# Kernel optimization log

Hardware: AMD Instinct MI355X
Metric: run time of the kernel (lower is better)

The kernel has to match this reference:

```python
import jax, jax.numpy as jnp
import numpy as np

B, S, D = 4, 4096, 768
E, SLOTS = 16, 1  # n_experts, slots_per_expert
H = 4 * D


def setup_inputs() -> dict:
    key = jax.random.key(0)
    k = jax.random.split(key, 6)
    scale1 = 1.0 / np.sqrt(D)
    scale2 = 1.0 / np.sqrt(H)
    return {
        "x": jax.random.normal(k[0], (B, S, D), dtype=jnp.float32),
        "phi": jax.random.normal(k[1], (D, E * SLOTS), dtype=jnp.float32),
        "W1": jax.random.normal(k[2], (E, D, H), dtype=jnp.float32) * scale1,
        "b1": jnp.zeros((E, H), dtype=jnp.float32),
        "W2": jax.random.normal(k[3], (E, H, D), dtype=jnp.float32) * scale2,
        "b2": jnp.zeros((E, D), dtype=jnp.float32),
    }


def reference(x, phi, W1, b1, W2, b2):
    # logits: [B, S, E*SLOTS]
    logits = jnp.einsum("bsd,dn->bsn", x, phi)
    dispatch_weights = jax.nn.softmax(logits, axis=-1)  # over slots
    combine_weights = jax.nn.softmax(logits, axis=1)    # over sequence
    # xs: [B, E*SLOTS, D] = dispatch^T @ x
    xs = jnp.einsum("bsn,bsd->bnd", dispatch_weights, x)
    xs = xs.reshape(B, E, SLOTS, D)
    # per-expert FFN, batched over experts: GELU (exact, as torch nn.GELU default)
    h = jnp.einsum("bepd,edh->beph", xs, W1) + b1[None, :, None, :]
    h = jax.nn.gelu(h, approximate=False)
    ys = jnp.einsum("beph,ehd->bepd", h, W2) + b2[None, :, None, :]
    ys = ys.reshape(B, E * SLOTS, D)
    # combine: [B, S, D]
    y = jnp.einsum("bsn,bnd->bsd", combine_weights, ys)
    return y
```

## Files before the change

kernel.cpp:

```cpp
#include <hip/hip_runtime.h>
#include <math.h>

constexpr int B = 4, S = 4096, D = 768, E = 16, N = 16, H = 3072;
constexpr int SCH = 32;
constexpr int NSCH = S / SCH;
constexpr int DL = 24;
constexpr int NDC = D / DL;
constexpr int HL2 = 96;
constexpr int NHC2 = H / HL2;
constexpr int LBLK = 32;
constexpr int LPB = S / LBLK;

constexpr size_t OFF_LOG  = 0;
constexpr size_t OFF_DW   = OFF_LOG + (size_t)B * S * N;
constexpr size_t OFF_PCM  = OFF_DW + (size_t)B * S * N;
constexpr size_t OFF_PCS  = OFF_PCM + (size_t)B * LPB * N;
constexpr size_t OFF_CMAX = OFF_PCS + (size_t)B * LPB * N;
constexpr size_t OFF_CSUM = OFF_CMAX + (size_t)B * N;
constexpr size_t OFF_XSP  = OFF_CSUM + (size_t)B * N;
constexpr size_t OFF_XS   = OFF_XSP + (size_t)B * NSCH * N * D;
constexpr size_t OFF_HP   = OFF_XS + (size_t)B * N * D;
constexpr size_t OFF_HACT = OFF_HP + (size_t)NDC * B * E * H;
constexpr size_t OFF_YSP  = OFF_HACT + (size_t)B * E * H;
constexpr size_t OFF_YS   = OFF_YSP + (size_t)NHC2 * B * E * D;

__device__ __forceinline__ void fma4(float4& a, float s, const float4& w) {
    a.x = fmaf(s, w.x, a.x);
    a.y = fmaf(s, w.y, a.y);
    a.z = fmaf(s, w.z, a.z);
    a.w = fmaf(s, w.w, a.w);
}

__global__ __launch_bounds__(256) void k_logits(const float* __restrict__ x,
                                                const float* __restrict__ phi,
                                                float* __restrict__ logits,
                                                float* __restrict__ dw,
                                                float* __restrict__ pcm,
                                                float* __restrict__ pcs) {
    __shared__ float ph[16][D];
    __shared__ float rm[16][16], rs[16][16];
    const int t = threadIdx.x;
    const int blk = blockIdx.x;
    const int b = blk / LPB;
    const int s0 = (blk % LPB) * LBLK;

#pragma unroll
    for (int i = 0; i < 12; ++i) {
        const int idx = i * 1024 + t * 4;
        const float4 v = *reinterpret_cast<const float4*>(phi + idx);
        const int d0 = idx >> 4;
        const int n0 = idx & 15;
        ph[n0 + 0][d0] = v.x;
        ph[n0 + 1][d0] = v.y;
        ph[n0 + 2][d0] = v.z;
        ph[n0 + 3][d0] = v.w;
    }
    __syncthreads();

    const int gid = t >> 4;
    const int ln = t & 15;
    const int s = s0 + gid * 2;
    const float* xr0 = x + ((size_t)b * S + s) * D;
    const float* xr1 = xr0 + D;

    float4 a0[12], a1[12];
#pragma unroll
    for (int j = 0; j < 12; ++j) {
        a0[j] = *reinterpret_cast<const float4*>(xr0 + j * 64 + ln * 4);
        a1[j] = *reinterpret_cast<const float4*>(xr1 + j * 64 + ln * 4);
    }
    float p0[16], p1[16];
#pragma unroll
    for (int n = 0; n < 16; ++n) {
        float q0 = 0.f, q1 = 0.f;
#pragma unroll
        for (int j = 0; j < 12; ++j) {
            const float4 pv = *reinterpret_cast<const float4*>(&ph[n][j * 64 + ln * 4]);
            q0 = fmaf(a0[j].x, pv.x, q0); q1 = fmaf(a1[j].x, pv.x, q1);
            q0 = fmaf(a0[j].y, pv.y, q0); q1 = fmaf(a1[j].y, pv.y, q1);
            q0 = fmaf(a0[j].z, pv.z, q0); q1 = fmaf(a1[j].z, pv.z, q1);
            q0 = fmaf(a0[j].w, pv.w, q0); q1 = fmaf(a1[j].w, pv.w, q1);
        }
        p0[n] = q0; p1[n] = q1;
    }
#pragma unroll
    for (int m = 1; m < 16; m <<= 1) {
#pragma unroll
        for (int n = 0; n < 16; ++n) {
            p0[n] += __shfl_xor(p0[n], m, 64);
            p1[n] += __shfl_xor(p1[n], m, 64);
        }
    }
    float m0 = -1e30f, m1 = -1e30f;
#pragma unroll
    for (int n = 0; n < 16; ++n) { m0 = fmaxf(m0, p0[n]); m1 = fmaxf(m1, p1[n]); }
    float su0 = 0.f, su1 = 0.f;
#pragma unroll
    for (int n = 0; n < 16; ++n) { su0 += __expf(p0[n] - m0); su1 += __expf(p1[n] - m1); }
    const size_t o0 = ((size_t)b * S + s) * N + ln;
    logits[o0] = p0[ln];
    logits[o0 + N] = p1[ln];
    dw[o0] = __expf(p0[ln] - m0) / su0;
    dw[o0 + N] = __expf(p1[ln] - m1) / su1;

    const float mm = fmaxf(p0[ln], p1[ln]);
    const float ss = __expf(p0[ln] - mm) + __expf(p1[ln] - mm);
    rm[gid][ln] = mm;
    rs[gid][ln] = ss;
    __syncthreads();
    if (t < 16) {
        float M = -1e30f;
#pragma unroll
        for (int g = 0; g < 16; ++g) M = fmaxf(M, rm[g][t]);
        float SS = 0.f;
#pragma unroll
        for (int g = 0; g < 16; ++g) SS += rs[g][t] * __expf(rm[g][t] - M);
        pcm[blk * 16 + t] = M;
        pcs[blk * 16 + t] = SS;
    }
}

__global__ __launch_bounds__(192) void k_xsp(const float* __restrict__ x,
                                             const float* __restrict__ dw,
                                             float* __restrict__ xsp) {
    const int blk = blockIdx.x;
    const int b = blk / NSCH;
    const int c = blk % NSCH;
    const int t = threadIdx.x;
    const int d = t * 4;
    float4 a[16];
#pragma unroll
    for (int n = 0; n < 16; ++n) a[n] = float4{0.f, 0.f, 0.f, 0.f};
    const float* xb = x + ((size_t)b * S + (size_t)c * SCH) * D + d;
    const float* dwb = dw + ((size_t)b * S + (size_t)c * SCH) * N;
#pragma unroll 2
    for (int s = 0; s < SCH; ++s) {
        const float4 xv = *reinterpret_cast<const float4*>(xb + (size_t)s * D);
#pragma unroll
        for (int n = 0; n < 16; ++n) {
            const float w = dwb[s * N + n];
            a[n].x = fmaf(w, xv.x, a[n].x);
            a[n].y = fmaf(w, xv.y, a[n].y);
            a[n].z = fmaf(w, xv.z, a[n].z);
            a[n].w = fmaf(w, xv.w, a[n].w);
        }
    }
    float* o = xsp + (size_t)blk * N * D + d;
#pragma unroll
    for (int n = 0; n < 16; ++n)
        *reinterpret_cast<float4*>(o + (size_t)n * D) = a[n];
}

__global__ __launch_bounds__(256) void k_xsred_cmerge(const float* __restrict__ xsp,
                                                      float* __restrict__ xs,
                                                      const float* __restrict__ pcm,
                                                      const float* __restrict__ pcs,
                                                      float* __restrict__ cmax,
                                                      float* __restrict__ csum) {
    const int t = threadIdx.x;
    if (blockIdx.x < 192) {
        const int i = blockIdx.x * 256 + t;
        const int b = i / (N * D);
        const int rem = i % (N * D);
        const float* p = xsp + (size_t)b * NSCH * N * D + rem;
        float sum = 0.f;
#pragma unroll 4
        for (int c = 0; c < NSCH; ++c) sum += p[(size_t)c * N * D];
        xs[i] = sum;
    } else if (t < 64) {
        const int b = t >> 4, n = t & 15;
        float M = -1e30f;
#pragma unroll 8
        for (int c = 0; c < LPB; ++c) M = fmaxf(M, pcm[((size_t)b * LPB + c) * 16 + n]);
        float SS = 0.f;
#pragma unroll 8
        for (int c = 0; c < LPB; ++c)
            SS += pcs[((size_t)b * LPB + c) * 16 + n] * __expf(pcm[((size_t)b * LPB + c) * 16 + n] - M);
        cmax[b * 16 + n] = M;
        csum[b * 16 + n] = SS;
    }
}

__global__ __launch_bounds__(256) void k_ffn1(const float* __restrict__ xs,
                                              const float* __restrict__ W1,
                                              float* __restrict__ hp) {
    __shared__ __align__(16) float xs_lds[DL][4];
    const int t = threadIdx.x;
    const int e = blockIdx.x / NDC;
    const int dc = blockIdx.x % NDC;
    const int d0 = dc * DL;
    if (t < DL * 4) {
        const int dd = t >> 2, b = t & 3;
        xs_lds[dd][b] = xs[((size_t)b * N + e) * D + d0 + dd];
    }
    __syncthreads();

    float4 acc[3][4];
#pragma unroll
    for (int k = 0; k < 3; ++k)
#pragma unroll
        for (int b = 0; b < 4; ++b) acc[k][b] = float4{0.f, 0.f, 0.f, 0.f};

    const float* wbase = W1 + ((size_t)e * D + d0) * H + t * 4;
#pragma unroll 4
    for (int dd = 0; dd < DL; ++dd) {
        const float4 xv = *reinterpret_cast<const float4*>(&xs_lds[dd][0]);
        const float* wrow = wbase + (size_t)dd * H;
        float4 w[3];
        w[0] = *reinterpret_cast<const float4*>(wrow);
        w[1] = *reinterpret_cast<const float4*>(wrow + 1024);
        w[2] = *reinterpret_cast<const float4*>(wrow + 2048);
#pragma unroll
        for (int k = 0; k < 3; ++k) {
            fma4(acc[k][0], xv.x, w[k]);
            fma4(acc[k][1], xv.y, w[k]);
            fma4(acc[k][2], xv.z, w[k]);
            fma4(acc[k][3], xv.w, w[k]);
        }
    }
#pragma unroll
    for (int k = 0; k < 3; ++k)
#pragma unroll
        for (int b = 0; b < 4; ++b)
            *reinterpret_cast<float4*>(hp + (((size_t)dc * 4 + b) * E + e) * H + k * 1024 + t * 4) = acc[k][b];
}

__global__ __launch_bounds__(256) void k_gelu(const float* __restrict__ hp,
                                              const float* __restrict__ b1,
                                              float* __restrict__ hact) {
    const int i4 = blockIdx.x * 256 + threadIdx.x;
    const int rem4 = i4 % (E * H / 4);
    float4 v = *reinterpret_cast<const float4*>(b1 + (size_t)rem4 * 4);
#pragma unroll 8
    for (int dc = 0; dc < NDC; ++dc) {
        const float4 p = *reinterpret_cast<const float4*>(hp + (size_t)dc * B * E * H + (size_t)i4 * 4);
        v.x += p.x; v.y += p.y; v.z += p.z; v.w += p.w;
    }
    float4 g;
    g.x = 0.5f * v.x * (1.0f + erff(v.x * 0.70710678118654752f));
    g.y = 0.5f * v.y * (1.0f + erff(v.y * 0.70710678118654752f));
    g.z = 0.5f * v.z * (1.0f + erff(v.z * 0.70710678118654752f));
    g.w = 0.5f * v.w * (1.0f + erff(v.w * 0.70710678118654752f));
    *reinterpret_cast<float4*>(hact + (size_t)i4 * 4) = g;
}

__global__ __launch_bounds__(192) void k_ffn2(const float* __restrict__ hact,
                                              const float* __restrict__ W2,
                                              float* __restrict__ ysp) {
    __shared__ __align__(16) float h_lds[HL2][4];
    const int t = threadIdx.x;
    const int e = blockIdx.x / NHC2;
    const int hc = blockIdx.x % NHC2;
    const int h0 = hc * HL2;
    for (int idx = t; idx < HL2 * 4; idx += 192) {
        const int hh = idx >> 2, b = idx & 3;
        h_lds[hh][b] = hact[((size_t)b * E + e) * H + h0 + hh];
    }
    __syncthreads();

    float4 acc[4];
#pragma unroll
    for (int b = 0; b < 4; ++b) acc[b] = float4{0.f, 0.f, 0.f, 0.f};

    const float* wbase = W2 + ((size_t)e * H + h0) * D + t * 4;
#pragma unroll 8
    for (int kk = 0; kk < HL2; ++kk) {
        const float4 hv = *reinterpret_cast<const float4*>(&h_lds[kk][0]);
        const float4 w = *reinterpret_cast<const float4*>(wbase + (size_t)kk * D);
        fma4(acc[0], hv.x, w);
        fma4(acc[1], hv.y, w);
        fma4(acc[2], hv.z, w);
        fma4(acc[3], hv.w, w);
    }
#pragma unroll
    for (int b = 0; b < 4; ++b)
        *reinterpret_cast<float4*>(ysp + (((size_t)hc * 4 + b) * E + e) * D + t * 4) = acc[b];
}

__global__ __launch_bounds__(256) void k_ysred(const float* __restrict__ ysp,
                                               const float* __restrict__ b2,
                                               float* __restrict__ ys) {
    const int i4 = blockIdx.x * 256 + threadIdx.x;
    const int rem4 = i4 % (E * D / 4);
    float4 v = *reinterpret_cast<const float4*>(b2 + (size_t)rem4 * 4);
#pragma unroll 8
    for (int hc = 0; hc < NHC2; ++hc) {
        const float4 u = *reinterpret_cast<const float4*>(ysp + (size_t)hc * B * E * D + (size_t)i4 * 4);
        v.x += u.x; v.y += u.y; v.z += u.z; v.w += u.w;
    }
    *reinterpret_cast<float4*>(ys + (size_t)i4 * 4) = v;
}

__global__ __launch_bounds__(192) void k_combine(const float* __restrict__ logits,
                                                 const float* __restrict__ cmax,
                                                 const float* __restrict__ csum,
                                                 const float* __restrict__ ys,
                                                 float* __restrict__ y) {
    const int blk = blockIdx.x;
    const int b = blk / (S / 8);
    const int s0 = (blk % (S / 8)) * 8;
    const int t = threadIdx.x;
    const int d4 = t * 4;

    float4 ysr[16];
    float cm[16], ci[16];
#pragma unroll
    for (int n = 0; n < 16; ++n) {
        ysr[n] = *reinterpret_cast<const float4*>(ys + ((size_t)b * N + n) * D + d4);
        cm[n] = cmax[b * N + n];
        ci[n] = 1.0f / csum[b * N + n];
    }
#pragma unroll
    for (int r = 0; r < 8; ++r) {
        const int s = s0 + r;
        const float* lrow = logits + ((size_t)b * S + s) * N;
        float4 acc{0, 0, 0, 0};
#pragma unroll
        for (int n = 0; n < 16; ++n) {
            const float cw = __expf(lrow[n] - cm[n]) * ci[n];
            acc.x = fmaf(cw, ysr[n].x, acc.x);
            acc.y = fmaf(cw, ysr[n].y, acc.y);
            acc.z = fmaf(cw, ysr[n].z, acc.z);
            acc.w = fmaf(cw, ysr[n].w, acc.w);
        }
        *reinterpret_cast<float4*>(y + ((size_t)b * S + s) * D + d4) = acc;
    }
}

extern "C" void kernel_launch(void* const* d_in, const int* in_sizes, int n_in,
                              void* d_out, int out_size, void* d_ws, size_t ws_size,
                              hipStream_t stream) {
    const float* x   = (const float*)d_in[0];
    const float* phi = (const float*)d_in[1];
    const float* W1  = (const float*)d_in[2];
    const float* b1  = (const float*)d_in[3];
    const float* W2  = (const float*)d_in[4];
    const float* b2  = (const float*)d_in[5];
    float* y = (float*)d_out;
    float* ws = (float*)d_ws;

    float* logits = ws + OFF_LOG;
    float* dw     = ws + OFF_DW;
    float* pcm    = ws + OFF_PCM;
    float* pcs    = ws + OFF_PCS;
    float* cmax   = ws + OFF_CMAX;
    float* csum   = ws + OFF_CSUM;
    float* xsp    = ws + OFF_XSP;
    float* xs     = ws + OFF_XS;
    float* hp     = ws + OFF_HP;
    float* hact   = ws + OFF_HACT;
    float* ysp    = ws + OFF_YSP;
    float* ys     = ws + OFF_YS;

    k_logits<<<B * LPB, 256, 0, stream>>>(x, phi, logits, dw, pcm, pcs);
    k_xsp<<<B * NSCH, 192, 0, stream>>>(x, dw, xsp);
    k_xsred_cmerge<<<193, 256, 0, stream>>>(xsp, xs, pcm, pcs, cmax, csum);
    k_ffn1<<<E * NDC, 256, 0, stream>>>(xs, W1, hp);
    k_gelu<<<(B * E * H / 4) / 256, 256, 0, stream>>>(hp, b1, hact);
    k_ffn2<<<E * NHC2, 192, 0, stream>>>(hact, W2, ysp);
    k_ysred<<<(B * E * D / 4) / 256, 256, 0, stream>>>(ysp, b2, ys);
    k_combine<<<B * (S / 8), 192, 0, stream>>>(logits, cmax, csum, ys, y);
}
```

Before: 171.2 us.

## Fuse hidden partial-sum reduction and GELU into FFN2, retile FFN1 over columns

Removes the standalone GELU kernel by having each FFN2 block reduce the FFN1 partial sums for its hidden slice, add the bias, apply exact GELU and stage the result in LDS. FFN1 now splits each expert's hidden columns into three blocks and uses a larger D chunk, so there are fewer partial sums to reduce and each thread holds fewer accumulators. FFN2 uses a smaller hidden chunk, which means more blocks and more ys partials, and the ys reduction loop is unrolled further. This saves a launch and the hact write/read round trip, but the hp partials are now read inside FFN2 and the ysp reduction has twice as much to sum.

```diff
diff --git a/kernel.cpp b/kernel.cpp
--- a/kernel.cpp
+++ b/kernel.cpp
@@ -4,9 +4,10 @@
 constexpr int B = 4, S = 4096, D = 768, E = 16, N = 16, H = 3072;
 constexpr int SCH = 32;
 constexpr int NSCH = S / SCH;
-constexpr int DL = 24;
-constexpr int NDC = D / DL;
-constexpr int HL2 = 96;
+constexpr int DL1 = 48;
+constexpr int NDC = D / DL1;
+constexpr int NHH = 3;
+constexpr int HL2 = 48;
 constexpr int NHC2 = H / HL2;
 constexpr int LBLK = 32;
 constexpr int LPB = S / LBLK;
@@ -20,8 +21,7 @@
 constexpr size_t OFF_XSP  = OFF_CSUM + (size_t)B * N;
 constexpr size_t OFF_XS   = OFF_XSP + (size_t)B * NSCH * N * D;
 constexpr size_t OFF_HP   = OFF_XS + (size_t)B * N * D;
-constexpr size_t OFF_HACT = OFF_HP + (size_t)NDC * B * E * H;
-constexpr size_t OFF_YSP  = OFF_HACT + (size_t)B * E * H;
+constexpr size_t OFF_YSP  = OFF_HP + (size_t)NDC * B * E * H;
 constexpr size_t OFF_YS   = OFF_YSP + (size_t)NHC2 * B * E * D;
 
 __device__ __forceinline__ void fma4(float4& a, float s, const float4& w) {
@@ -184,77 +184,59 @@
 __global__ __launch_bounds__(256) void k_ffn1(const float* __restrict__ xs,
                                               const float* __restrict__ W1,
                                               float* __restrict__ hp) {
-    __shared__ __align__(16) float xs_lds[DL][4];
-    const int t = threadIdx.x;
-    const int e = blockIdx.x / NDC;
-    const int dc = blockIdx.x % NDC;
-    const int d0 = dc * DL;
-    if (t < DL * 4) {
+    __shared__ __align__(16) float xs_lds[DL1][4];
+    const int t = threadIdx.x;
+    const int e = blockIdx.x / (NDC * NHH);
+    const int rem = blockIdx.x % (NDC * NHH);
+    const int dc = rem / NHH;
+    const int hh = rem % NHH;
+    const int d0 = dc * DL1;
+    const int col = hh * 1024 + t * 4;
+
+    if (t < DL1 * 4) {
         const int dd = t >> 2, b = t & 3;
         xs_lds[dd][b] = xs[((size_t)b * N + e) * D + d0 + dd];
     }
     __syncthreads();
 
-    float4 acc[3][4];
-#pragma unroll
-    for (int k = 0; k < 3; ++k)
-#pragma unroll
-        for (int b = 0; b < 4; ++b) acc[k][b] = float4{0.f, 0.f, 0.f, 0.f};
-
-    const float* wbase = W1 + ((size_t)e * D + d0) * H + t * 4;
-#pragma unroll 4
-    for (int dd = 0; dd < DL; ++dd) {
+    float4 acc[4];
+#pragma unroll
+    for (int b = 0; b < 4; ++b) acc[b] = float4{0.f, 0.f, 0.f, 0.f};
+
+    const float* wp = W1 + ((size_t)e * D + d0) * H + col;
+#pragma unroll 8
+    for (int dd = 0; dd < DL1; ++dd) {
+        const float4 w = *reinterpret_cast<const float4*>(wp + (size_t)dd * H);
         const float4 xv = *reinterpret_cast<const float4*>(&xs_lds[dd][0]);
-        const float* wrow = wbase + (size_t)dd * H;
-        float4 w[3];
-        w[0] = *reinterpret_cast<const float4*>(wrow);
-        w[1] = *reinterpret_cast<const float4*>(wrow + 1024);
-        w[2] = *reinterpret_cast<const float4*>(wrow + 2048);
-#pragma unroll
-        for (int k = 0; k < 3; ++k) {
-            fma4(acc[k][0], xv.x, w[k]);
-            fma4(acc[k][1], xv.y, w[k]);
-            fma4(acc[k][2], xv.z, w[k]);
-            fma4(acc[k][3], xv.w, w[k]);
-        }
-    }
-#pragma unroll
-    for (int k = 0; k < 3; ++k)
-#pragma unroll
-        for (int b = 0; b < 4; ++b)
-            *reinterpret_cast<float4*>(hp + (((size_t)dc * 4 + b) * E + e) * H + k * 1024 + t * 4) = acc[k][b];
-}
-
-__global__ __launch_bounds__(256) void k_gelu(const float* __restrict__ hp,
+        fma4(acc[0], xv.x, w);
+        fma4(acc[1], xv.y, w);
+        fma4(acc[2], xv.z, w);
+        fma4(acc[3], xv.w, w);
+    }
+#pragma unroll
+    for (int b = 0; b < 4; ++b)
+        *reinterpret_cast<float4*>(hp + (((size_t)dc * 4 + b) * E + e) * H + col) = acc[b];
+}
+
+__global__ __launch_bounds__(192) void k_ffn2(const float* __restrict__ hp,
                                               const float* __restrict__ b1,
-                                              float* __restrict__ hact) {
-    const int i4 = blockIdx.x * 256 + threadIdx.x;
-    const int rem4 = i4 % (E * H / 4);
-    float4 v = *reinterpret_cast<const float4*>(b1 + (size_t)rem4 * 4);
-#pragma unroll 8
-    for (int dc = 0; dc < NDC; ++dc) {
-        const float4 p = *reinterpret_cast<const float4*>(hp + (size_t)dc * B * E * H + (size_t)i4 * 4);
-        v.x += p.x; v.y += p.y; v.z += p.z; v.w += p.w;
-    }
-    float4 g;
-    g.x = 0.5f * v.x * (1.0f + erff(v.x * 0.70710678118654752f));
-    g.y = 0.5f * v.y * (1.0f + erff(v.y * 0.70710678118654752f));
-    g.z = 0.5f * v.z * (1.0f + erff(v.z * 0.70710678118654752f));
-    g.w = 0.5f * v.w * (1.0f + erff(v.w * 0.70710678118654752f));
-    *reinterpret_cast<float4*>(hact + (size_t)i4 * 4) = g;
-}
-
-__global__ __launch_bounds__(192) void k_ffn2(const float* __restrict__ hact,
                                               const float* __restrict__ W2,
                                               float* __restrict__ ysp) {
-    __shared__ __align__(16) float h_lds[HL2][4];
+    __shared__ __align__(16) float g_lds[HL2][4];
     const int t = threadIdx.x;
     const int e = blockIdx.x / NHC2;
     const int hc = blockIdx.x % NHC2;
     const int h0 = hc * HL2;
-    for (int idx = t; idx < HL2 * 4; idx += 192) {
-        const int hh = idx >> 2, b = idx & 3;
-        h_lds[hh][b] = hact[((size_t)b * E + e) * H + h0 + hh];
+
+    {
+        const int b = t / HL2;
+        const int hh = t % HL2;
+        float v = b1[(size_t)e * H + h0 + hh];
+#pragma unroll
+        for (int dc = 0; dc < NDC; ++dc)
+            v += hp[(((size_t)dc * 4 + b) * E + e) * H + h0 + hh];
+        v = 0.5f * v * (1.0f + erff(v * 0.70710678118654752f));
+        g_lds[hh][b] = v;
     }
     __syncthreads();
 
@@ -262,11 +244,11 @@
 #pragma unroll
     for (int b = 0; b < 4; ++b) acc[b] = float4{0.f, 0.f, 0.f, 0.f};
 
-    const float* wbase = W2 + ((size_t)e * H + h0) * D + t * 4;
+    const float* wp = W2 + ((size_t)e * H + h0) * D + t * 4;
 #pragma unroll 8
     for (int kk = 0; kk < HL2; ++kk) {
-        const float4 hv = *reinterpret_cast<const float4*>(&h_lds[kk][0]);
-        const float4 w = *reinterpret_cast<const float4*>(wbase + (size_t)kk * D);
+        const float4 w = *reinterpret_cast<const float4*>(wp + (size_t)kk * D);
+        const float4 hv = *reinterpret_cast<const float4*>(&g_lds[kk][0]);
         fma4(acc[0], hv.x, w);
         fma4(acc[1], hv.y, w);
         fma4(acc[2], hv.z, w);
@@ -283,7 +265,7 @@
     const int i4 = blockIdx.x * 256 + threadIdx.x;
     const int rem4 = i4 % (E * D / 4);
     float4 v = *reinterpret_cast<const float4*>(b2 + (size_t)rem4 * 4);
-#pragma unroll 8
+#pragma unroll 16
     for (int hc = 0; hc < NHC2; ++hc) {
         const float4 u = *reinterpret_cast<const float4*>(ysp + (size_t)hc * B * E * D + (size_t)i4 * 4);
         v.x += u.x; v.y += u.y; v.z += u.z; v.w += u.w;
@@ -348,16 +330,14 @@
     float* xsp    = ws + OFF_XSP;
     float* xs     = ws + OFF_XS;
     float* hp     = ws + OFF_HP;
-    float* hact   = ws + OFF_HACT;
     float* ysp    = ws + OFF_YSP;
     float* ys     = ws + OFF_YS;
 
     k_logits<<<B * LPB, 256, 0, stream>>>(x, phi, logits, dw, pcm, pcs);
     k_xsp<<<B * NSCH, 192, 0, stream>>>(x, dw, xsp);
     k_xsred_cmerge<<<193, 256, 0, stream>>>(xsp, xs, pcm, pcs, cmax, csum);
-    k_ffn1<<<E * NDC, 256, 0, stream>>>(xs, W1, hp);
-    k_gelu<<<(B * E * H / 4) / 256, 256, 0, stream>>>(hp, b1, hact);
-    k_ffn2<<<E * NHC2, 192, 0, stream>>>(hact, W2, ysp);
+    k_ffn1<<<E * NDC * NHH, 256, 0, stream>>>(xs, W1, hp);
+    k_ffn2<<<E * NHC2, 192, 0, stream>>>(hp, b1, W2, ysp);
     k_ysred<<<(B * E * D / 4) / 256, 256, 0, stream>>>(ysp, b2, ys);
     k_combine<<<B * (S / 8), 192, 0, stream>>>(logits, cmax, csum, ys, y);
 }
```

Result: faster. 164.5 us (-3.9%).
